# Kernel optimization log

Hardware: AMD Instinct MI355X
Metric: run time of the kernel (lower is better)

Reference implementation:

```python
import jax, jax.numpy as jnp
import numpy as np

B, S, H = 2, 1024, 2048
D = 256          # index_dimension = min(index.embedding_dimension, hidden_size)
R = 32           # LoRA rank
K = 4            # index_k neighbors per query token
N_DB = 100000    # rows in the external index


def setup_inputs() -> dict:
    key = jax.random.key(0)
    ks = jax.random.split(key, 7)
    return {
        "hidden_states": jax.random.normal(ks[0], (B, S, H), jnp.float32),
        "db_keys": jax.random.normal(ks[1], (N_DB, D), jnp.float32),
        "db_values": jax.random.normal(ks[2], (N_DB, D), jnp.float32),
        "wq_in": jax.random.normal(ks[3], (H, R), jnp.float32) * 0.02,
        "wq_out": jax.random.normal(ks[4], (R, D), jnp.float32) * 0.02,
        "wv_in": jax.random.normal(ks[5], (D, R), jnp.float32) * 0.02,
        "wv_out": jax.random.normal(ks[6], (R, H), jnp.float32) * 0.02,
    }


def reference(hidden_states, db_keys, db_values, wq_in, wq_out, wv_in, wv_out):
    b, s, h = hidden_states.shape
    d = wq_out.shape[1]
    # query LoRA projection: hidden -> r -> index_dim
    q = (hidden_states @ wq_in) @ wq_out            # [B, S, D]

    # external k-NN lookup (exact L2 top-k over index table), no_grad in torch
    qf = q.reshape(b * s, d)                        # [B*S, D]
    qn = jnp.sum(qf * qf, axis=-1, keepdims=True)   # [B*S, 1]
    kn = jnp.sum(db_keys * db_keys, axis=-1)        # [N_DB]
    dist = qn - 2.0 * (qf @ db_keys.T) + kn[None, :]  # [B*S, N_DB]
    _, idx = jax.lax.top_k(-dist, K)                # [B*S, K] nearest neighbors

    # gather KV and reshape to [B, S*K, D] (matches torch view calls)
    kv_key = jax.lax.stop_gradient(db_keys[idx]).reshape(b, s * K, d)
    kv_val = jax.lax.stop_gradient(db_values[idx]).reshape(b, s * K, d)

    # SDPA, is_causal=True with Lq != Lk: top-left aligned tril mask (j <= i)
    scale = 1.0 / np.sqrt(d).astype(np.float32)
    scores = jnp.einsum('bqd,bkd->bqk', q, kv_key) * scale  # [B, S, S*K]
    mask = jnp.arange(s * K)[None, :] <= jnp.arange(s)[:, None]
    scores = jnp.where(mask[None, :, :], scores, jnp.finfo(scores.dtype).min)
    attn = jax.nn.softmax(scores, axis=-1)
    out = jnp.einsum('bqk,bkd->bqd', attn, kv_val)  # [B, S, D]

    # value LoRA projection: index_dim -> r -> hidden
    return (out @ wv_in) @ wv_out                   # [B, S, H]
```

## Files before the change

kernel.cpp:

```cpp
#include <hip/hip_runtime.h>
#include <cfloat>

#define B_   2
#define S_   1024
#define H_   2048
#define D_   256
#define R_   32
#define K_   4
#define NDB_ 100000

#define TSEL 256
#define NSEL (B_ * TSEL)

#define NCHUNK     61
#define CHUNK_ROWS 1664
#define TILES      13
#define NT         128
#define MT         64
#define KC         64
#define LSTR       68

#define NEG_INF  (-3.0e38f)
#define IDX_MAX  0x7fffffff

#define TQ 4

#define OFF_Q     0
#define OFF_KN    0x200000
#define OFF_PS    0x280000
#define OFF_PI    0x300000
#define OFF_IDX   0x380000
#define OFF_CAND  0x3A0000
#define OFF_KVT   0x400000
#define OFF_AO    0x600000
#define OFF_KVV   0x800000
#define OFF_DBK16 0xA00000

typedef unsigned short ushort_t;
typedef unsigned int   uint_t;
typedef __attribute__((ext_vector_type(8)))  __bf16 bf16x8;
typedef __attribute__((ext_vector_type(16))) float  f32x16;

__device__ __forceinline__ void ins4(float sc, int n, float s[4], int id[4]) {
  if (sc > s[3] || (sc == s[3] && n < id[3])) {
    s[3] = sc; id[3] = n;
#pragma unroll
    for (int k = 3; k > 0; --k) {
      if (s[k] > s[k - 1] || (s[k] == s[k - 1] && id[k] < id[k - 1])) {
        float ts = s[k]; s[k] = s[k - 1]; s[k - 1] = ts;
        int ti = id[k]; id[k] = id[k - 1]; id[k - 1] = ti;
      }
    }
  }
}

__device__ __forceinline__ uint_t bfpack(float a, float b) {
  uint_t ua = __float_as_uint(a), ub = __float_as_uint(b);
  ua = (ua + 0x7fffu + ((ua >> 16) & 1u)) >> 16;
  ub = (ub + 0x7fffu + ((ub >> 16) & 1u)) >> 16;
  return ua | (ub << 16);
}

__global__ __launch_bounds__(256) void k_compute_q(
    const float* __restrict__ hidden, const float* __restrict__ wq_in,
    const float* __restrict__ wq_out, float* __restrict__ q) {
  __shared__ float hrow[H_];
  __shared__ float part[8][R_];
  __shared__ float q1[R_];
  const int m = blockIdx.x;
  const int t = threadIdx.x;
  const float* hp = hidden + (size_t)m * H_;
  ((float4*)hrow)[t]       = ((const float4*)hp)[t];
  ((float4*)hrow)[t + 256] = ((const float4*)hp)[t + 256];
  __syncthreads();
  const int r = t & 31, c = t >> 5;
  float p = 0.f;
#pragma unroll 4
  for (int e = c * 256; e < c * 256 + 256; ++e)
    p = fmaf(hrow[e], wq_in[(size_t)e * R_ + r], p);
  part[c][r] = p;
  __syncthreads();
  if (t < R_) {
    float s = 0.f;
#pragma unroll
    for (int cc = 0; cc < 8; ++cc) s += part[cc][t];
    q1[t] = s;
  }
  __syncthreads();
  float acc = 0.f;
#pragma unroll
  for (int rr = 0; rr < R_; ++rr) acc = fmaf(q1[rr], wq_out[rr * D_ + t], acc);
  q[(size_t)m * D_ + t] = acc;
}

__global__ __launch_bounds__(256) void k_kn_cvt(const float* __restrict__ dbk,
                                               float* __restrict__ kn,
                                               ushort_t* __restrict__ dbk16) {
  const int w = threadIdx.x >> 6, l = threadIdx.x & 63;
  const int n = blockIdx.x * 4 + w;
  if (n >= NDB_) return;
  const float4 v = ((const float4*)(dbk + (size_t)n * D_))[l];
  uint2 p; p.x = bfpack(v.x, v.y); p.y = bfpack(v.z, v.w);
  ((uint2*)(dbk16 + (size_t)n * D_))[l] = p;
  float s = v.x * v.x + v.y * v.y + v.z * v.z + v.w * v.w;
#pragma unroll
  for (int off = 32; off; off >>= 1) s += __shfl_down(s, off);
  if (l == 0) kn[n] = s;
}

__global__ __launch_bounds__(256) void k_kn(const float* __restrict__ dbk,
                                            float* __restrict__ kn) {
  const int w = threadIdx.x >> 6, l = threadIdx.x & 63;
  const int n = blockIdx.x * 4 + w;
  if (n >= NDB_) return;
  const float4 v = ((const float4*)(dbk + (size_t)n * D_))[l];
  float s = v.x * v.x + v.y * v.y + v.z * v.z + v.w * v.w;
#pragma unroll
  for (int off = 32; off; off >>= 1) s += __shfl_down(s, off);
  if (l == 0) kn[n] = s;
}

__global__ __launch_bounds__(256, 2) void k_knn_mfma(
    const float* __restrict__ q, const ushort_t* __restrict__ dbk16,
    const float* __restrict__ kn, float* __restrict__ pscore,
    int* __restrict__ pidx) {
  __shared__ __align__(16) char smem[65536];
  ushort_t* sA = (ushort_t*)smem;
  ushort_t* sB = (ushort_t*)(smem + 32768);
  float*    sS = (float*)(smem + 32768);

  const int fid = blockIdx.x;
  const int chunk = (fid & 7) + 8 * ((fid >> 3) & 7);
  const int qb = fid >> 6;
  if (chunk >= NCHUNK) return;

  const int tid = threadIdx.x;
  const int wv = tid >> 6, ln = tid & 63;
  const int lm = ln & 31, lh = ln >> 5;
  const int tx = tid & 15, ty = tid >> 4;
  const int row_base = chunk * CHUNK_ROWS;

  {
    const int m = tid & 63, cg = tid >> 6;
    const int sq = qb * MT + m;
    const float* qp = q + ((size_t)((sq >> 8) * S_ + (sq & 255))) * D_;
#pragma unroll
    for (int cc = 0; cc < 8; ++cc) {
      const int c = cg * 8 + cc;
      const float4 v0 = *(const float4*)(qp + c * 8);
      const float4 v1 = *(const float4*)(qp + c * 8 + 4);
      uint4 pk;
      pk.x = bfpack(v0.x, v0.y); pk.y = bfpack(v0.z, v0.w);
      pk.z = bfpack(v1.x, v1.y); pk.w = bfpack(v1.z, v1.w);
      *(uint4*)&sA[(m * 32 + (c ^ (m & 7))) * 8] = pk;
    }
  }

  float s4[4][4]; int i4[4][4];
#pragma unroll
  for (int a = 0; a < 4; ++a)
#pragma unroll
    for (int b = 0; b < 4; ++b) { s4[a][b] = NEG_INF; i4[a][b] = IDX_MAX; }

  for (int tile = 0; tile < TILES; ++tile) {
    const int row0 = row_base + tile * NT;
    if (row0 >= NDB_) break;

    f32x16 acc0, acc1;
#pragma unroll
    for (int r = 0; r < 16; ++r) { acc0[r] = 0.f; acc1[r] = 0.f; }

    for (int kh = 0; kh < 2; ++kh) {
      __syncthreads();
      {
        const int n_in = ln >> 4;
        const int p    = ln & 15;
#pragma unroll
        for (int i = 0; i < 8; ++i) {
          const int nloc = wv * 32 + i * 4 + n_in;
          int krow = row0 + nloc; if (krow >= NDB_) krow = NDB_ - 1;
          const int c = p ^ (nloc & 7);
          const ushort_t* gp = dbk16 + (size_t)krow * D_ + (kh * 16 + c) * 8;
          ushort_t* lp = sB + (size_t)(wv * 32 + i * 4) * 128;
          __builtin_amdgcn_global_load_lds(
              (const __attribute__((address_space(1))) void*)gp,
              (__attribute__((address_space(3))) void*)lp, 16, 0, 0);
        }
      }
      __syncthreads();
      const int nB = wv * 32 + lm;
      const int bswz = nB & 7;
#pragma unroll
      for (int ks = 0; ks < 8; ++ks) {
        const int cA = kh * 16 + ks * 2 + lh;
        const bf16x8 a0 = *(const bf16x8*)&sA[(lm * 32 + (cA ^ (lm & 7))) * 8];
        const bf16x8 a1 = *(const bf16x8*)&sA[((32 + lm) * 32 + (cA ^ (lm & 7))) * 8];
        const bf16x8 bb = *(const bf16x8*)&sB[(nB * 16 + ((ks * 2 + lh) ^ bswz)) * 8];
        acc0 = __builtin_amdgcn_mfma_f32_32x32x16_bf16(a0, bb, acc0, 0, 0, 0);
        acc1 = __builtin_amdgcn_mfma_f32_32x32x16_bf16(a1, bb, acc1, 0, 0, 0);
      }
    }
    __syncthreads();

    {
      const int n = (tid >> 6) * 32 + lm;
#pragma unroll
      for (int r = 0; r < 16; ++r) {
        const int mrow = (r & 3) + 8 * (r >> 2) + 4 * lh;
        sS[mrow * 128 + n]        = acc0[r];
        sS[(32 + mrow) * 128 + n] = acc1[r];
      }
    }
    __syncthreads();

    {
      const int nbase = row0 + tx * 8;
      float knv[8]; int nok[8];
#pragma unroll
      for (int j = 0; j < 8; ++j) {
        nok[j] = (nbase + j < NDB_);
        knv[j] = nok[j] ? kn[nbase + j] : 0.f;
      }
#pragma unroll
      for (int qi = 0; qi < 4; ++qi) {
        const int m = ty * 4 + qi;
        const float4 v0 = *(const float4*)&sS[m * 128 + tx * 8];
        const float4 v1 = *(const float4*)&sS[m * 128 + tx * 8 + 4];
        const float sv[8] = {v0.x, v0.y, v0.z, v0.w, v1.x, v1.y, v1.z, v1.w};
        float v[8];
#pragma unroll
        for (int j = 0; j < 8; ++j)
          v[j] = nok[j] ? fmaf(2.f, sv[j], -knv[j]) : NEG_INF;
        const float mx = fmaxf(fmaxf(fmaxf(v[0], v[1]), fmaxf(v[2], v[3])),
                               fmaxf(fmaxf(v[4], v[5]), fmaxf(v[6], v[7])));
        if (mx >= s4[qi][3]) {
#pragma unroll
          for (int j = 0; j < 8; ++j)
            if (nok[j]) ins4(v[j], nbase + j, s4[qi], i4[qi]);
        }
      }
    }
  }

  __syncthreads();
  float* cs = (float*)smem;
  int*   ci = (int*)(smem + 64 * 65 * 4);
#pragma unroll
  for (int qi = 0; qi < 4; ++qi)
#pragma unroll
    for (int k = 0; k < 4; ++k) {
      cs[(ty * 4 + qi) * 65 + tx * 4 + k] = s4[qi][k];
      ci[(ty * 4 + qi) * 65 + tx * 4 + k] = i4[qi][k];
    }
  __syncthreads();
  if (tid < 64) {
    float fs[4]; int fi[4];
#pragma unroll
    for (int k = 0; k < 4; ++k) { fs[k] = NEG_INF; fi[k] = IDX_MAX; }
    for (int c = 0; c < 64; ++c)
      ins4(cs[tid * 65 + c], ci[tid * 65 + c], fs, fi);
    const int sq = qb * MT + tid;
    float* po = pscore + ((size_t)sq * NCHUNK + chunk) * 4;
    int*   io = pidx   + ((size_t)sq * NCHUNK + chunk) * 4;
#pragma unroll
    for (int k = 0; k < 4; ++k) { po[k] = fs[k]; io[k] = fi[k]; }
  }
}

__global__ __launch_bounds__(256) void k_knn_partial(
    const float* __restrict__ q, const float* __restrict__ dbk,
    const float* __restrict__ kn, float* __restrict__ pscore,
    int* __restrict__ pidx) {
  __shared__ float smem[3 * KC * LSTR];
  float* sA  = smem;
  float* sB0 = smem + KC * LSTR;
  float* sB1 = smem + 2 * KC * LSTR;
  const int tid = threadIdx.x;
  const int tx = tid & 15, ty = tid >> 4;
  const int chunk = blockIdx.x, qb = blockIdx.y;
  const int arq = tid >> 2;
  const int aqd = (tid & 3) * 4;
  const int brk = tid >> 1;
  const int bh  = tid & 1;
  const int bcol = ((brk >> 3) << 2) | (brk & 3);
  float* sBw = (brk & 4) ? sB1 : sB0;
  const int sq_a = qb * MT + arq;
  const float* qsrc = q + ((size_t)((sq_a >> 8) * S_ + (sq_a & 255))) * D_;
  float s4[4][4]; int i4[4][4];
#pragma unroll
  for (int a = 0; a < 4; ++a)
#pragma unroll
    for (int b = 0; b < 4; ++b) { s4[a][b] = NEG_INF; i4[a][b] = IDX_MAX; }
  const int row_base = chunk * CHUNK_ROWS;
  for (int tile = 0; tile < TILES; ++tile) {
    const int row0 = row_base + tile * NT;
    if (row0 >= NDB_) break;
    int krow = row0 + brk; if (krow >= NDB_) krow = NDB_ - 1;
    const float* ksrc = dbk + (size_t)krow * D_;
    float acc[4][8];
#pragma unroll
    for (int a = 0; a < 4; ++a)
#pragma unroll
      for (int b = 0; b < 8; ++b) acc[a][b] = 0.f;
    for (int kc = 0; kc < 4; ++kc) {
      __syncthreads();
#pragma unroll
      for (int p = 0; p < 4; ++p) {
        const int kkl = p * 16 + aqd;
        const float4 v = *(const float4*)(qsrc + kc * KC + kkl);
        sA[(kkl + 0) * LSTR + arq] = v.x;
        sA[(kkl + 1) * LSTR + arq] = v.y;
        sA[(kkl + 2) * LSTR + arq] = v.z;
        sA[(kkl + 3) * LSTR + arq] = v.w;
      }
#pragma unroll
      for (int p = 0; p < 8; ++p) {
        const int kkl = bh * 32 + p * 4;
        const float4 v = *(const float4*)(ksrc + kc * KC + kkl);
        sBw[(kkl + 0) * LSTR + bcol] = v.x;
        sBw[(kkl + 1) * LSTR + bcol] = v.y;
        sBw[(kkl + 2) * LSTR + bcol] = v.z;
        sBw[(kkl + 3) * LSTR + bcol] = v.w;
      }
      __syncthreads();
#pragma unroll 4
      for (int kk = 0; kk < KC; ++kk) {
        const float4 a  = *(const float4*)&sA [kk * LSTR + ty * 4];
        const float4 b0 = *(const float4*)&sB0[kk * LSTR + tx * 4];
        const float4 b1 = *(const float4*)&sB1[kk * LSTR + tx * 4];
        const float av[4] = {a.x, a.y, a.z, a.w};
        const float bv[8] = {b0.x, b0.y, b0.z, b0.w, b1.x, b1.y, b1.z, b1.w};
#pragma unroll
        for (int qi = 0; qi < 4; ++qi)
#pragma unroll
          for (int nj = 0; nj < 8; ++nj)
            acc[qi][nj] = fmaf(av[qi], bv[nj], acc[qi][nj]);
      }
    }
#pragma unroll
    for (int nj = 0; nj < 8; ++nj) {
      const int n = row0 + tx * 8 + nj;
      if (n < NDB_) {
        const float knj = kn[n];
        ins4(2.f * acc[0][nj] - knj, n, s4[0], i4[0]);
        ins4(2.f * acc[1][nj] - knj, n, s4[1], i4[1]);
        ins4(2.f * acc[2][nj] - knj, n, s4[2], i4[2]);
        ins4(2.f * acc[3][nj] - knj, n, s4[3], i4[3]);
      }
    }
  }
  __syncthreads();
  float* cs = smem;
  int*   ci = (int*)(smem + 64 * 65);
#pragma unroll
  for (int qi = 0; qi < 4; ++qi)
#pragma unroll
    for (int k = 0; k < 4; ++k) {
      cs[(ty * 4 + qi) * 65 + tx * 4 + k] = s4[qi][k];
      ci[(ty * 4 + qi) * 65 + tx * 4 + k] = i4[qi][k];
    }
  __syncthreads();
  if (tid < 64) {
    float fs[4]; int fi[4];
#pragma unroll
    for (int k = 0; k < 4; ++k) { fs[k] = NEG_INF; fi[k] = IDX_MAX; }
    for (int c = 0; c < 64; ++c)
      ins4(cs[tid * 65 + c], ci[tid * 65 + c], fs, fi);
    const int sq = qb * MT + tid;
    float* po = pscore + ((size_t)sq * NCHUNK + chunk) * 4;
    int*   io = pidx   + ((size_t)sq * NCHUNK + chunk) * 4;
#pragma unroll
    for (int k = 0; k < 4; ++k) { po[k] = fs[k]; io[k] = fi[k]; }
  }
}

template <int RANKS>
__device__ __forceinline__ void merge_top(const float* __restrict__ pscore,
                                          const int* __restrict__ pidx,
                                          int* __restrict__ outp) {
  const int sq = blockIdx.x, l = threadIdx.x;
  float s4[4]; int i4[4];
#pragma unroll
  for (int k = 0; k < 4; ++k) { s4[k] = NEG_INF; i4[k] = IDX_MAX; }
  for (int c = l; c < NCHUNK * 4; c += 64)
    ins4(pscore[(size_t)sq * NCHUNK * 4 + c], pidx[(size_t)sq * NCHUNK * 4 + c], s4, i4);
#pragma unroll
  for (int r = 0; r < RANKS; ++r) {
    float s = s4[0]; int i = i4[0];
#pragma unroll
    for (int off = 32; off; off >>= 1) {
      float so = __shfl_down(s, off); int io = __shfl_down(i, off);
      if (so > s || (so == s && io < i)) { s = so; i = io; }
    }
    const float sw = __shfl(s, 0); const int iw = __shfl(i, 0);
    if (l == 0) outp[sq * RANKS + r] = iw;
    if (s4[0] == sw && i4[0] == iw) {
      s4[0] = s4[1]; i4[0] = i4[1];
      s4[1] = s4[2]; i4[1] = i4[2];
      s4[2] = s4[3]; i4[2] = i4[3];
      s4[3] = NEG_INF; i4[3] = IDX_MAX;
    }
  }
}

__global__ __launch_bounds__(64) void k_knn_merge4(const float* __restrict__ ps,
                                                   const int* __restrict__ pi,
                                                   int* __restrict__ knn_idx) {
  merge_top<4>(ps, pi, knn_idx);
}
__global__ __launch_bounds__(64) void k_knn_merge16(const float* __restrict__ ps,
                                                    const int* __restrict__ pi,
                                                    int* __restrict__ cand) {
  merge_top<16>(ps, pi, cand);
}

__global__ __launch_bounds__(256) void k_rescore(const float* __restrict__ q,
                                                 const float* __restrict__ dbk,
                                                 const float* __restrict__ kn,
                                                 const int* __restrict__ cand,
                                                 int* __restrict__ knn_idx) {
  __shared__ float scs[16];
  __shared__ int   sci[16];
  const int sq = blockIdx.x, wv = threadIdx.x >> 6, l = threadIdx.x & 63;
  const float* qp = q + ((size_t)((sq >> 8) * S_ + (sq & 255))) * D_;
  const float4 qv = ((const float4*)qp)[l];
  for (int cc = wv; cc < 16; cc += 4) {
    const int n = cand[sq * 16 + cc];
    const float4 kv = ((const float4*)(dbk + (size_t)n * D_))[l];
    float s = qv.x * kv.x + qv.y * kv.y + qv.z * kv.z + qv.w * kv.w;
#pragma unroll
    for (int off = 32; off; off >>= 1) s += __shfl_down(s, off);
    if (l == 0) { scs[cc] = 2.f * s - kn[n]; sci[cc] = n; }
  }
  __syncthreads();
  if (threadIdx.x == 0) {
    float s4[4]; int i4[4];
#pragma unroll
    for (int k = 0; k < 4; ++k) { s4[k] = NEG_INF; i4[k] = IDX_MAX; }
#pragma unroll
    for (int c = 0; c < 16; ++c) ins4(scs[c], sci[c], s4, i4);
#pragma unroll
    for (int k = 0; k < 4; ++k) knn_idx[sq * 4 + k] = i4[k];
  }
}

__global__ __launch_bounds__(256) void k_gather(const float* __restrict__ dbk,
                                                const float* __restrict__ dbv,
                                                const int* __restrict__ knn_idx,
                                                float* __restrict__ kvT,
                                                float* __restrict__ kvV) {
  const int b = blockIdx.x >> 6, j0 = (blockIdx.x & 63) * 16;
  const int w = threadIdx.x >> 6, l = threadIdx.x & 63;
  float* dstT = kvT + (size_t)b * D_ * 1024;
  float* dstV = kvV + (size_t)b * 1024 * D_;
  for (int jj = w; jj < 16; jj += 4) {
    const int j = j0 + jj;
    const int row = knn_idx[b * 1024 + j];
    const float4 kv = ((const float4*)(dbk + (size_t)row * D_))[l];
    dstT[(4 * l + 0) * 1024 + j] = kv.x;
    dstT[(4 * l + 1) * 1024 + j] = kv.y;
    dstT[(4 * l + 2) * 1024 + j] = kv.z;
    dstT[(4 * l + 3) * 1024 + j] = kv.w;
    const float4 vv = ((const float4*)(dbv + (size_t)row * D_))[l];
    ((float4*)(dstV + (size_t)j * D_))[l] = vv;
  }
}

template <int CMAX>
__device__ __forceinline__ void qk_dots(const float* __restrict__ kb, int t,
                                        const float (*qrow)[D_], float a[4][TQ]) {
#pragma unroll 2
  for (int d = 0; d < D_; d += 4) {
    float qv[TQ][4];
#pragma unroll
    for (int q = 0; q < TQ; ++q) {
      const float4 v = *(const float4*)&qrow[q][d];
      qv[q][0] = v.x; qv[q][1] = v.y; qv[q][2] = v.z; qv[q][3] = v.w;
    }
#pragma unroll
    for (int dd = 0; dd < 4; ++dd) {
      float kv[CMAX];
#pragma unroll
      for (int c = 0; c < CMAX; ++c)
        kv[c] = kb[(size_t)(d + dd) * 1024 + c * 256 + t];
#pragma unroll
      for (int c = 0; c < CMAX; ++c)
#pragma unroll
        for (int q = 0; q < TQ; ++q)
          a[c][q] = fmaf(qv[q][dd], kv[c], a[c][q]);
    }
  }
}

__global__ __launch_bounds__(256) void k_attn(const float* __restrict__ qarr,
                                              const float* __restrict__ kvT,
                                              const float* __restrict__ kvV,
                                              float* __restrict__ attout) {
  __shared__ float qrow[TQ][D_];
  __shared__ float attw[TQ][1024];
  __shared__ float pvred[4][TQ][D_];
  __shared__ float redm[4][TQ], reds[4][TQ];

  const int fid = blockIdx.x;
  const int b = fid & 1;
  const int g = fid >> 1;
  const int h = g >> 1;
  const int grp = (g & 1) ? (255 - h) : h;
  const int i0 = grp * TQ;
  const int t = threadIdx.x;
  const int w = t >> 6, l = t & 63;
  const int nkmax = i0 + TQ;
  const int cmax = (nkmax + 255) >> 8;

  {
    const float4 v = ((const float4*)(qarr + ((size_t)b * S_ + i0 + w) * D_))[l];
    float4 sv;
    sv.x = v.x * 0.0625f; sv.y = v.y * 0.0625f;
    sv.z = v.z * 0.0625f; sv.w = v.w * 0.0625f;
    ((float4*)&qrow[w][0])[l] = sv;
  }
  __syncthreads();

  const float* kb = kvT + (size_t)b * D_ * 1024;
  float a[4][TQ];
#pragma unroll
  for (int c = 0; c < 4; ++c)
#pragma unroll
    for (int q = 0; q < TQ; ++q) a[c][q] = 0.f;
  switch (cmax) {
    case 1: qk_dots<1>(kb, t, qrow, a); break;
    case 2: qk_dots<2>(kb, t, qrow, a); break;
    case 3: qk_dots<3>(kb, t, qrow, a); break;
    default: qk_dots<4>(kb, t, qrow, a); break;
  }
#pragma unroll
  for (int c = 0; c < 4; ++c)
    if (c < cmax)
#pragma unroll
      for (int q = 0; q < TQ; ++q)
        if (c * 256 + t > i0 + q) a[c][q] = NEG_INF;

  float M[TQ];
#pragma unroll
  for (int q = 0; q < TQ; ++q) {
    float m = NEG_INF;
    for (int c = 0; c < cmax; ++c) m = fmaxf(m, a[c][q]);
#pragma unroll
    for (int off = 32; off; off >>= 1) m = fmaxf(m, __shfl_down(m, off));
    if (l == 0) redm[w][q] = m;
  }
  __syncthreads();
#pragma unroll
  for (int q = 0; q < TQ; ++q)
    M[q] = fmaxf(fmaxf(redm[0][q], redm[1][q]), fmaxf(redm[2][q], redm[3][q]));
  float inv[TQ];
#pragma unroll
  for (int q = 0; q < TQ; ++q) {
    float s = 0.f;
    for (int c = 0; c < cmax; ++c) {
      const float p = (a[c][q] > 0.5f * NEG_INF) ? __expf(a[c][q] - M[q]) : 0.f;
      a[c][q] = p; s += p;
    }
#pragma unroll
    for (int off = 32; off; off >>= 1) s += __shfl_down(s, off);
    if (l == 0) reds[w][q] = s;
  }
  __syncthreads();
#pragma unroll
  for (int q = 0; q < TQ; ++q)
    inv[q] = 1.f / (reds[0][q] + reds[1][q] + reds[2][q] + reds[3][q]);
  for (int c = 0; c < cmax; ++c)
#pragma unroll
    for (int q = 0; q < TQ; ++q)
      attw[q][c * 256 + t] = a[c][q] * inv[q];
  __syncthreads();

  const float* vb = kvV + (size_t)b * 1024 * D_;
  float4 acc[TQ];
#pragma unroll
  for (int q = 0; q < TQ; ++q) acc[q] = make_float4(0.f, 0.f, 0.f, 0.f);
#pragma unroll 2
  for (int j = w; j < nkmax; j += 4) {
    const float4 v = ((const float4*)(vb + (size_t)j * D_))[l];
#pragma unroll
    for (int q = 0; q < TQ; ++q) {
      const float p = attw[q][j];
      acc[q].x = fmaf(p, v.x, acc[q].x);
      acc[q].y = fmaf(p, v.y, acc[q].y);
      acc[q].z = fmaf(p, v.z, acc[q].z);
      acc[q].w = fmaf(p, v.w, acc[q].w);
    }
  }
#pragma unroll
  for (int q = 0; q < TQ; ++q) ((float4*)&pvred[w][q][0])[l] = acc[q];
  __syncthreads();
  {
    const int q = t >> 6;
    float4 s = make_float4(0.f, 0.f, 0.f, 0.f);
#pragma unroll
    for (int ww = 0; ww < 4; ++ww) {
      const float4 p = ((const float4*)&pvred[ww][q][0])[l];
      s.x += p.x; s.y += p.y; s.z += p.z; s.w += p.w;
    }
    ((float4*)(attout + ((size_t)b * S_ + i0 + q) * D_))[l] = s;
  }
}

__global__ __launch_bounds__(256) void k_out(const float* __restrict__ attout,
                                             const float* __restrict__ wv_in,
                                             const float* __restrict__ wv_out,
                                             float* __restrict__ y) {
  __shared__ float row[D_];
  __shared__ float part[8][R_];
  __shared__ float t32[R_];
  const int m = blockIdx.x, t = threadIdx.x;
  row[t] = attout[(size_t)m * D_ + t];
  __syncthreads();
  const int r = t & 31, c = t >> 5;
  float p = 0.f;
#pragma unroll
  for (int d = c * 32; d < c * 32 + 32; ++d)
    p = fmaf(row[d], wv_in[d * R_ + r], p);
  part[c][r] = p;
  __syncthreads();
  if (t < R_) {
    float s = 0.f;
#pragma unroll
    for (int cc = 0; cc < 8; ++cc) s += part[cc][t];
    t32[t] = s;
  }
  __syncthreads();
  for (int hh = t; hh < H_; hh += 256) {
    float a = 0.f;
#pragma unroll
    for (int rr = 0; rr < R_; ++rr) a = fmaf(t32[rr], wv_out[rr * H_ + hh], a);
    y[(size_t)m * H_ + hh] = a;
  }
}

extern "C" void kernel_launch(void* const* d_in, const int* in_sizes, int n_in,
                              void* d_out, int out_size, void* d_ws, size_t ws_size,
                              hipStream_t stream) {
  const float* hidden  = (const float*)d_in[0];
  const float* db_keys = (const float*)d_in[1];
  const float* db_vals = (const float*)d_in[2];
  const float* wq_in   = (const float*)d_in[3];
  const float* wq_out  = (const float*)d_in[4];
  const float* wv_in   = (const float*)d_in[5];
  const float* wv_out  = (const float*)d_in[6];
  float* out = (float*)d_out;

  char* ws = (char*)d_ws;
  float*    q      = (float*)(ws + OFF_Q);
  float*    kn     = (float*)(ws + OFF_KN);
  float*    ps     = (float*)(ws + OFF_PS);
  int*      pi     = (int*)  (ws + OFF_PI);
  int*      idx    = (int*)  (ws + OFF_IDX);
  int*      cand   = (int*)  (ws + OFF_CAND);
  float*    kvT    = (float*)(ws + OFF_KVT);
  float*    attout = (float*)(ws + OFF_AO);
  float*    kvV    = (float*)(ws + OFF_KVV);
  ushort_t* dbk16  = (ushort_t*)(ws + OFF_DBK16);

  const size_t need = (size_t)OFF_DBK16 + (size_t)NDB_ * D_ * 2;

  k_compute_q<<<B_ * S_, 256, 0, stream>>>(hidden, wq_in, wq_out, q);
  if (ws_size >= need) {
    k_kn_cvt<<<(NDB_ + 3) / 4, 256, 0, stream>>>(db_keys, kn, dbk16);
    k_knn_mfma<<<512, 256, 0, stream>>>(q, dbk16, kn, ps, pi);
    k_knn_merge16<<<NSEL, 64, 0, stream>>>(ps, pi, cand);
    k_rescore<<<NSEL, 256, 0, stream>>>(q, db_keys, kn, cand, idx);
  } else {
    k_kn<<<(NDB_ + 3) / 4, 256, 0, stream>>>(db_keys, kn);
    k_knn_partial<<<dim3(NCHUNK, 8), 256, 0, stream>>>(q, db_keys, kn, ps, pi);
    k_knn_merge4<<<NSEL, 64, 0, stream>>>(ps, pi, idx);
  }
  k_gather<<<2 * 64, 256, 0, stream>>>(db_keys, db_vals, idx, kvT, kvV);
  k_attn<<<512, 256, 0, stream>>>(q, kvT, kvV, attout);
  k_out<<<B_ * S_, 256, 0, stream>>>(attout, wv_in, wv_out, out);
}
```

Baseline: 495.7 us.

## Pre-swizzle bf16 keys into MFMA fragment layout and score directly from registers

The key conversion kernel now writes bf16 keys in a tiled layout that matches the MFMA operand fragment. The kNN kernel can then load B operands straight from global memory with no LDS staging and no per-tile barriers. Top-4 selection now works directly on the accumulator registers, with two per-lane candidate lists, instead of round-tripping scores through shared memory. Key norms are staged once per chunk in LDS. This removes LDS traffic and synchronisation from the hot loop, at the cost of direct global loads with less latency hiding, and a cross-lane merge that depends on the new layout.

```diff
diff --git a/kernel.cpp b/kernel.cpp
--- a/kernel.cpp
+++ b/kernel.cpp
@@ -93,19 +93,32 @@
   q[(size_t)m * D_ + t] = acc;
 }
 
-__global__ __launch_bounds__(256) void k_kn_cvt(const float* __restrict__ dbk,
-                                               float* __restrict__ kn,
-                                               ushort_t* __restrict__ dbk16) {
-  const int w = threadIdx.x >> 6, l = threadIdx.x & 63;
-  const int n = blockIdx.x * 4 + w;
-  if (n >= NDB_) return;
-  const float4 v = ((const float4*)(dbk + (size_t)n * D_))[l];
-  uint2 p; p.x = bfpack(v.x, v.y); p.y = bfpack(v.z, v.w);
-  ((uint2*)(dbk16 + (size_t)n * D_))[l] = p;
-  float s = v.x * v.x + v.y * v.y + v.z * v.z + v.w * v.w;
-#pragma unroll
-  for (int off = 32; off; off >>= 1) s += __shfl_down(s, off);
-  if (l == 0) kn[n] = s;
+__global__ __launch_bounds__(256) void k_kn_cvtT(const float* __restrict__ dbk,
+                                                 float* __restrict__ kn,
+                                                 ushort_t* __restrict__ dbk16T) {
+  const int n32 = blockIdx.x;
+  const int t = threadIdx.x;
+  const int r = t >> 3, tc = t & 7;
+  const int n = n32 * 32 + r;
+  const float* rp = dbk + (size_t)n * D_ + tc * 32;
+  uint4* dst = (uint4*)dbk16T;
+  float s = 0.f;
+#pragma unroll
+  for (int cc = 0; cc < 4; ++cc) {
+    const int c = tc * 4 + cc;
+    const float4 a = ((const float4*)rp)[cc * 2];
+    const float4 b = ((const float4*)rp)[cc * 2 + 1];
+    uint4 pk;
+    pk.x = bfpack(a.x, a.y); pk.y = bfpack(a.z, a.w);
+    pk.z = bfpack(b.x, b.y); pk.w = bfpack(b.z, b.w);
+    dst[(size_t)(n32 * 16 + (c >> 1)) * 64 + (c & 1) * 32 + r] = pk;
+    s += a.x*a.x + a.y*a.y + a.z*a.z + a.w*a.w;
+    s += b.x*b.x + b.y*b.y + b.z*b.z + b.w*b.w;
+  }
+  s += __shfl_down(s, 4, 8);
+  s += __shfl_down(s, 2, 8);
+  s += __shfl_down(s, 1, 8);
+  if (tc == 0) kn[n] = s;
 }
 
 __global__ __launch_bounds__(256) void k_kn(const float* __restrict__ dbk,
@@ -121,13 +134,12 @@
 }
 
 __global__ __launch_bounds__(256, 2) void k_knn_mfma(
-    const float* __restrict__ q, const ushort_t* __restrict__ dbk16,
+    const float* __restrict__ q, const ushort_t* __restrict__ dbk16T,
     const float* __restrict__ kn, float* __restrict__ pscore,
     int* __restrict__ pidx) {
-  __shared__ __align__(16) char smem[65536];
-  ushort_t* sA = (ushort_t*)smem;
-  ushort_t* sB = (ushort_t*)(smem + 32768);
-  float*    sS = (float*)(smem + 32768);
+  __shared__ __align__(16) char smem[32768 + CHUNK_ROWS * 4];
+  ushort_t* sA  = (ushort_t*)smem;
+  float*    knL = (float*)(smem + 32768);
 
   const int fid = blockIdx.x;
   const int chunk = (fid & 7) + 8 * ((fid >> 3) & 7);
@@ -137,7 +149,6 @@
   const int tid = threadIdx.x;
   const int wv = tid >> 6, ln = tid & 63;
   const int lm = ln & 31, lh = ln >> 5;
-  const int tx = tid & 15, ty = tid >> 4;
   const int row_base = chunk * CHUNK_ROWS;
 
   {
@@ -155,110 +166,95 @@
       *(uint4*)&sA[(m * 32 + (c ^ (m & 7))) * 8] = pk;
     }
   }
-
-  float s4[4][4]; int i4[4][4];
-#pragma unroll
-  for (int a = 0; a < 4; ++a)
-#pragma unroll
-    for (int b = 0; b < 4; ++b) { s4[a][b] = NEG_INF; i4[a][b] = IDX_MAX; }
+  for (int j = tid; j < CHUNK_ROWS; j += 256) {
+    int rr = row_base + j; if (rr >= NDB_) rr = NDB_ - 1;
+    knL[j] = kn[rr];
+  }
+  __syncthreads();
+
+  float s40[4], s41[4]; int i40[4], i41[4];
+#pragma unroll
+  for (int k = 0; k < 4; ++k) {
+    s40[k] = NEG_INF; i40[k] = IDX_MAX;
+    s41[k] = NEG_INF; i41[k] = IDX_MAX;
+  }
+
+  const int sw = lm & 7;
+  const int abase0 = lm * 32;
+  const int abase1 = (32 + lm) * 32;
+  const int nbase = wv * 32 + 4 * lh;
 
   for (int tile = 0; tile < TILES; ++tile) {
     const int row0 = row_base + tile * NT;
     if (row0 >= NDB_) break;
+    const int nw = row0 + wv * 32;
+    if (nw >= NDB_) continue;
 
     f32x16 acc0, acc1;
 #pragma unroll
     for (int r = 0; r < 16; ++r) { acc0[r] = 0.f; acc1[r] = 0.f; }
 
-    for (int kh = 0; kh < 2; ++kh) {
-      __syncthreads();
-      {
-        const int n_in = ln >> 4;
-        const int p    = ln & 15;
-#pragma unroll
-        for (int i = 0; i < 8; ++i) {
-          const int nloc = wv * 32 + i * 4 + n_in;
-          int krow = row0 + nloc; if (krow >= NDB_) krow = NDB_ - 1;
-          const int c = p ^ (nloc & 7);
-          const ushort_t* gp = dbk16 + (size_t)krow * D_ + (kh * 16 + c) * 8;
-          ushort_t* lp = sB + (size_t)(wv * 32 + i * 4) * 128;
-          __builtin_amdgcn_global_load_lds(
-              (const __attribute__((address_space(1))) void*)gp,
-              (__attribute__((address_space(3))) void*)lp, 16, 0, 0);
-        }
-      }
-      __syncthreads();
-      const int nB = wv * 32 + lm;
-      const int bswz = nB & 7;
-#pragma unroll
-      for (int ks = 0; ks < 8; ++ks) {
-        const int cA = kh * 16 + ks * 2 + lh;
-        const bf16x8 a0 = *(const bf16x8*)&sA[(lm * 32 + (cA ^ (lm & 7))) * 8];
-        const bf16x8 a1 = *(const bf16x8*)&sA[((32 + lm) * 32 + (cA ^ (lm & 7))) * 8];
-        const bf16x8 bb = *(const bf16x8*)&sB[(nB * 16 + ((ks * 2 + lh) ^ bswz)) * 8];
-        acc0 = __builtin_amdgcn_mfma_f32_32x32x16_bf16(a0, bb, acc0, 0, 0, 0);
-        acc1 = __builtin_amdgcn_mfma_f32_32x32x16_bf16(a1, bb, acc1, 0, 0, 0);
-      }
-    }
-    __syncthreads();
-
-    {
-      const int n = (tid >> 6) * 32 + lm;
-#pragma unroll
-      for (int r = 0; r < 16; ++r) {
-        const int mrow = (r & 3) + 8 * (r >> 2) + 4 * lh;
-        sS[mrow * 128 + n]        = acc0[r];
-        sS[(32 + mrow) * 128 + n] = acc1[r];
-      }
-    }
-    __syncthreads();
-
-    {
-      const int nbase = row0 + tx * 8;
-      float knv[8]; int nok[8];
-#pragma unroll
-      for (int j = 0; j < 8; ++j) {
-        nok[j] = (nbase + j < NDB_);
-        knv[j] = nok[j] ? kn[nbase + j] : 0.f;
-      }
-#pragma unroll
-      for (int qi = 0; qi < 4; ++qi) {
-        const int m = ty * 4 + qi;
-        const float4 v0 = *(const float4*)&sS[m * 128 + tx * 8];
-        const float4 v1 = *(const float4*)&sS[m * 128 + tx * 8 + 4];
-        const float sv[8] = {v0.x, v0.y, v0.z, v0.w, v1.x, v1.y, v1.z, v1.w};
-        float v[8];
-#pragma unroll
-        for (int j = 0; j < 8; ++j)
-          v[j] = nok[j] ? fmaf(2.f, sv[j], -knv[j]) : NEG_INF;
-        const float mx = fmaxf(fmaxf(fmaxf(v[0], v[1]), fmaxf(v[2], v[3])),
-                               fmaxf(fmaxf(v[4], v[5]), fmaxf(v[6], v[7])));
-        if (mx >= s4[qi][3]) {
-#pragma unroll
-          for (int j = 0; j < 8; ++j)
-            if (nok[j]) ins4(v[j], nbase + j, s4[qi], i4[qi]);
-        }
+    const ushort_t* gw = dbk16T + (size_t)(nw >> 5) * 8192 + (size_t)ln * 8;
+#pragma unroll
+    for (int ks = 0; ks < 16; ++ks) {
+      const bf16x8 bb = *(const bf16x8*)(gw + ks * 512);
+      const int cs = (2 * ks + lh) ^ sw;
+      const bf16x8 a0 = *(const bf16x8*)&sA[(abase0 + cs) * 8];
+      const bf16x8 a1 = *(const bf16x8*)&sA[(abase1 + cs) * 8];
+      acc0 = __builtin_amdgcn_mfma_f32_32x32x16_bf16(bb, a0, acc0, 0, 0, 0);
+      acc1 = __builtin_amdgcn_mfma_f32_32x32x16_bf16(bb, a1, acc1, 0, 0, 0);
+    }
+
+#pragma unroll
+    for (int g = 0; g < 4; ++g) {
+      float v0[4], v1[4]; int nn[4];
+#pragma unroll
+      for (int j = 0; j < 4; ++j) {
+        const int r = g * 4 + j;
+        const int off = (r & 3) + 8 * (r >> 2);
+        const int nloc = nbase + off;
+        const float knv = knL[tile * 128 + nloc];
+        const int n = row0 + nloc;
+        nn[j] = n;
+        const float x0 = fmaf(2.f, acc0[r], -knv);
+        const float x1 = fmaf(2.f, acc1[r], -knv);
+        const bool ok = n < NDB_;
+        v0[j] = ok ? x0 : NEG_INF;
+        v1[j] = ok ? x1 : NEG_INF;
+      }
+      const float m0 = fmaxf(fmaxf(v0[0], v0[1]), fmaxf(v0[2], v0[3]));
+      if (m0 >= s40[3]) {
+#pragma unroll
+        for (int j = 0; j < 4; ++j) ins4(v0[j], nn[j], s40, i40);
+      }
+      const float m1 = fmaxf(fmaxf(v1[0], v1[1]), fmaxf(v1[2], v1[3]));
+      if (m1 >= s41[3]) {
+#pragma unroll
+        for (int j = 0; j < 4; ++j) ins4(v1[j], nn[j], s41, i41);
       }
     }
   }
 
   __syncthreads();
   float* cs = (float*)smem;
-  int*   ci = (int*)(smem + 64 * 65 * 4);
-#pragma unroll
-  for (int qi = 0; qi < 4; ++qi)
+  int*   ci = (int*)(smem + 8192);
+  {
+    const int st = wv * 2 + lh;
 #pragma unroll
     for (int k = 0; k < 4; ++k) {
-      cs[(ty * 4 + qi) * 65 + tx * 4 + k] = s4[qi][k];
-      ci[(ty * 4 + qi) * 65 + tx * 4 + k] = i4[qi][k];
-    }
+      cs[(lm * 8 + st) * 4 + k]        = s40[k];
+      ci[(lm * 8 + st) * 4 + k]        = i40[k];
+      cs[((32 + lm) * 8 + st) * 4 + k] = s41[k];
+      ci[((32 + lm) * 8 + st) * 4 + k] = i41[k];
+    }
+  }
   __syncthreads();
   if (tid < 64) {
     float fs[4]; int fi[4];
 #pragma unroll
     for (int k = 0; k < 4; ++k) { fs[k] = NEG_INF; fi[k] = IDX_MAX; }
-    for (int c = 0; c < 64; ++c)
-      ins4(cs[tid * 65 + c], ci[tid * 65 + c], fs, fi);
+    for (int c = 0; c < 32; ++c)
+      ins4(cs[tid * 32 + c], ci[tid * 32 + c], fs, fi);
     const int sq = qb * MT + tid;
     float* po = pscore + ((size_t)sq * NCHUNK + chunk) * 4;
     int*   io = pidx   + ((size_t)sq * NCHUNK + chunk) * 4;
@@ -666,7 +662,7 @@
 
   k_compute_q<<<B_ * S_, 256, 0, stream>>>(hidden, wq_in, wq_out, q);
   if (ws_size >= need) {
-    k_kn_cvt<<<(NDB_ + 3) / 4, 256, 0, stream>>>(db_keys, kn, dbk16);
+    k_kn_cvtT<<<NDB_ / 32, 256, 0, stream>>>(db_keys, kn, dbk16);
     k_knn_mfma<<<512, 256, 0, stream>>>(q, dbk16, kn, ps, pi);
     k_knn_merge16<<<NSEL, 64, 0, stream>>>(ps, pi, cand);
     k_rescore<<<NSEL, 256, 0, stream>>>(q, db_keys, kn, cand, idx);
```

After: 451.6 us. 8.9% less time.
